# Kernel optimization log

Hardware: AMD Instinct MI355X
Metric: run time of the kernel (lower is better)

The kernel has to match this reference:

```python
import jax, jax.numpy as jnp
import numpy as np

NUM_INPUTS = 4096
K = 64
BATCH = 16384


def setup_inputs() -> dict:
    key = jax.random.key(0)
    X = jax.random.normal(key, (BATCH, NUM_INPUTS), dtype=jnp.float32)
    return {"X": X}


def reference(X):
    # Per-row (1 - k/n) quantile of |X| (linear interpolation, matching
    # torch.quantile default), then soft-threshold preserving sign.
    q = 1.0 - K / NUM_INPUTS
    X_abs = jnp.abs(X)
    Q = jnp.quantile(X_abs, q, axis=1, method="linear")  # [batch]
    X_trunc = jnp.maximum(X_abs - Q[:, None], 0.0)
    return jnp.sign(X) * X_trunc
```

## Files before the change

kernel.cpp:

```cpp
#include <hip/hip_runtime.h>
#include <cstdint>

constexpr int NCOLS   = 4096;
constexpr int THREADS = 256;
constexpr int EPT     = NCOLS / THREADS;
constexpr int KSEL    = 65;
constexpr uint32_t TPAT = 0x40000000u;
constexpr int CAP     = 256;

typedef float f32x4 __attribute__((ext_vector_type(4)));

__device__ __forceinline__ float soft(float x, float Q) {
    float r = fmaxf(fabsf(x) - Q, 0.0f);
    return copysignf(r, x);
}

__global__ __launch_bounds__(THREADS) void topk_sparsify(
    const float* __restrict__ X, float* __restrict__ out, int rows)
{
    const int row = blockIdx.x;
    if (row >= rows) return;
    const int t    = threadIdx.x;
    const int lane = t & 63;
    const int wave = t >> 6;

    const f32x4* __restrict__ x4 = reinterpret_cast<const f32x4*>(X + (size_t)row * NCOLS);
    f32x4* __restrict__       o4 = reinterpret_cast<f32x4*>(out + (size_t)row * NCOLS);

    f32x4 d[4];
#pragma unroll
    for (int i = 0; i < 4; ++i) d[i] = __builtin_nontemporal_load(x4 + t + THREADS * i);

    uint32_t a[EPT];
#pragma unroll
    for (int i = 0; i < 4; ++i) {
#pragma unroll
        for (int j = 0; j < 4; ++j)
            a[4 * i + j] = __float_as_uint(d[i][j]) & 0x7FFFFFFFu;
    }

    __shared__ uint32_t list[CAP];
    __shared__ uint32_t wtot[4];
    __shared__ uint32_t wcnt[4], wmn[4];
    __shared__ uint32_t b65_s;
    __shared__ float    q_sh;

    uint32_t cnt = 0;
#pragma unroll
    for (int i = 0; i < EPT; ++i) cnt += (a[i] > TPAT) ? 1u : 0u;

    uint32_t inc = cnt;
#pragma unroll
    for (int off = 1; off < 64; off <<= 1) {
        uint32_t v = __shfl_up(inc, off, 64);
        if (lane >= off) inc += v;
    }
    if (lane == 63) wtot[wave] = inc;
    __syncthreads();

    uint32_t C = 0, base = 0;
#pragma unroll
    for (int w = 0; w < 4; ++w) {
        uint32_t tw = wtot[w];
        C += tw;
        if (w < wave) base += tw;
    }
    const bool fast = (C >= (uint32_t)KSEL) && (C <= (uint32_t)CAP);

    if (fast) {
        uint32_t o = base + inc - cnt;
#pragma unroll
        for (int i = 0; i < EPT; ++i)
            if (a[i] > TPAT) list[o++] = a[i];
    }
    __syncthreads();

    uint32_t b65;
    if (fast) {
        if (t < 64) {
            const uint32_t c0 = ((uint32_t)t        < C) ? list[t]        : 0u;
            const uint32_t c1 = ((uint32_t)t + 64u  < C) ? list[t + 64]   : 0u;
            const uint32_t c2 = ((uint32_t)t + 128u < C) ? list[t + 128]  : 0u;
            const uint32_t c3 = ((uint32_t)t + 192u < C) ? list[t + 192]  : 0u;
            uint32_t prefix = 0, kk = KSEL;
            for (int b = 30; b >= 0; --b) {
                const uint32_t want = prefix | (1u << b);
                const uint32_t mhi  = ~((1u << b) - 1u);
                uint64_t m0 = __ballot((c0 & mhi) == want);
                uint64_t m1 = __ballot((c1 & mhi) == want);
                uint64_t m2 = __ballot((c2 & mhi) == want);
                uint64_t m3 = __ballot((c3 & mhi) == want);
                const uint32_t cc = (uint32_t)(__popcll(m0) + __popcll(m1) +
                                               __popcll(m2) + __popcll(m3));
                if (cc >= kk) prefix = want; else kk -= cc;
            }
            if (t == 0) b65_s = prefix;
        }
        __syncthreads();
        b65 = b65_s;
    } else {
        uint32_t prefix = 0, kk = KSEL;
        for (int b = 30; b >= 0; --b) {
            const uint32_t want = prefix | (1u << b);
            const uint32_t mhi  = ~((1u << b) - 1u);
            uint32_t c = 0;
#pragma unroll
            for (int i = 0; i < EPT; ++i) c += ((a[i] & mhi) == want) ? 1u : 0u;
#pragma unroll
            for (int off2 = 32; off2 >= 1; off2 >>= 1) c += __shfl_down(c, off2, 64);
            if (lane == 0) wcnt[wave] = c;
            __syncthreads();
            const uint32_t tot = wcnt[0] + wcnt[1] + wcnt[2] + wcnt[3];
            if (tot >= kk) prefix = want; else kk -= tot;
            __syncthreads();
        }
        b65 = prefix;
    }
    const float v65 = __uint_as_float(b65);

    uint32_t cgt = 0, mn = 0xFFFFFFFFu;
#pragma unroll
    for (int i = 0; i < EPT; ++i) {
        if (a[i] > b65) { cgt++; mn = min(mn, a[i]); }
    }
#pragma unroll
    for (int off2 = 32; off2 >= 1; off2 >>= 1) {
        cgt += __shfl_down(cgt, off2, 64);
        uint32_t m2 = __shfl_down(mn, off2, 64);
        mn = min(mn, m2);
    }
    if (lane == 0) { wcnt[wave] = cgt; wmn[wave] = mn; }
    __syncthreads();
    if (t == 0) {
        const uint32_t Ct = wcnt[0] + wcnt[1] + wcnt[2] + wcnt[3];
        const uint32_t M  = min(min(wmn[0], wmn[1]), min(wmn[2], wmn[3]));
        const float v64 = (Ct == 64u) ? __uint_as_float(M) : v65;
        q_sh = fmaf(0.015625f, v64 - v65, v65);
    }
    __syncthreads();
    const float Q = q_sh;

#pragma unroll
    for (int i = 0; i < 4; ++i) {
        f32x4 f;
#pragma unroll
        for (int j = 0; j < 4; ++j) f[j] = soft(d[i][j], Q);
        __builtin_nontemporal_store(f, o4 + t + THREADS * i);
    }
}

extern "C" void kernel_launch(void* const* d_in, const int* in_sizes, int n_in,
                              void* d_out, int out_size, void* d_ws, size_t ws_size,
                              hipStream_t stream) {
    const float* X   = (const float*)d_in[0];
    float*       out = (float*)d_out;
    const int rows = in_sizes[0] / NCOLS;
    topk_sparsify<<<rows, THREADS, 0, stream>>>(X, out, rows);
}
```

Measured before the change: 411.8 us.

## Drop raw input registers via sign bitmask and fold v64 search into fast path

Measured after the change: 410.6 us. About the same (-0.3%).

```diff
diff --git a/kernel.cpp b/kernel.cpp
--- a/kernel.cpp
+++ b/kernel.cpp
@@ -10,12 +10,7 @@
 
 typedef float f32x4 __attribute__((ext_vector_type(4)));
 
-__device__ __forceinline__ float soft(float x, float Q) {
-    float r = fmaxf(fabsf(x) - Q, 0.0f);
-    return copysignf(r, x);
-}
-
-__global__ __launch_bounds__(THREADS) void topk_sparsify(
+__global__ __launch_bounds__(THREADS, 8) void topk_sparsify(
     const float* __restrict__ X, float* __restrict__ out, int rows)
 {
     const int row = blockIdx.x;
@@ -25,24 +20,23 @@
     const int wave = t >> 6;
 
     const f32x4* __restrict__ x4 = reinterpret_cast<const f32x4*>(X + (size_t)row * NCOLS);
-    f32x4* __restrict__       o4 = reinterpret_cast<f32x4*>(out + (size_t)row * NCOLS);
-
-    f32x4 d[4];
-#pragma unroll
-    for (int i = 0; i < 4; ++i) d[i] = __builtin_nontemporal_load(x4 + t + THREADS * i);
 
     uint32_t a[EPT];
+    uint32_t smask = 0;
 #pragma unroll
     for (int i = 0; i < 4; ++i) {
+        f32x4 v = __builtin_nontemporal_load(x4 + t + THREADS * i);
 #pragma unroll
-        for (int j = 0; j < 4; ++j)
-            a[4 * i + j] = __float_as_uint(d[i][j]) & 0x7FFFFFFFu;
+        for (int j = 0; j < 4; ++j) {
+            const uint32_t p = __float_as_uint(v[j]);
+            smask |= (p >> 31) << (4 * i + j);
+            a[4 * i + j] = p & 0x7FFFFFFFu;
+        }
     }
 
     __shared__ uint32_t list[CAP];
     __shared__ uint32_t wtot[4];
     __shared__ uint32_t wcnt[4], wmn[4];
-    __shared__ uint32_t b65_s;
     __shared__ float    q_sh;
 
     uint32_t cnt = 0;
@@ -61,7 +55,7 @@
     uint32_t C = 0, base = 0;
 #pragma unroll
     for (int w = 0; w < 4; ++w) {
-        uint32_t tw = wtot[w];
+        const uint32_t tw = wtot[w];
         C += tw;
         if (w < wave) base += tw;
     }
@@ -72,33 +66,46 @@
 #pragma unroll
         for (int i = 0; i < EPT; ++i)
             if (a[i] > TPAT) list[o++] = a[i];
-    }
-    __syncthreads();
+        __syncthreads();
 
-    uint32_t b65;
-    if (fast) {
         if (t < 64) {
-            const uint32_t c0 = ((uint32_t)t        < C) ? list[t]        : 0u;
-            const uint32_t c1 = ((uint32_t)t + 64u  < C) ? list[t + 64]   : 0u;
-            const uint32_t c2 = ((uint32_t)t + 128u < C) ? list[t + 128]  : 0u;
-            const uint32_t c3 = ((uint32_t)t + 192u < C) ? list[t + 192]  : 0u;
+            const uint32_t c0 = ((uint32_t)t        < C) ? list[t]       : 0u;
+            const uint32_t c1 = ((uint32_t)t + 64u  < C) ? list[t + 64]  : 0u;
+            const uint32_t c2 = ((uint32_t)t + 128u < C) ? list[t + 128] : 0u;
+            const uint32_t c3 = ((uint32_t)t + 192u < C) ? list[t + 192] : 0u;
             uint32_t prefix = 0, kk = KSEL;
             for (int b = 30; b >= 0; --b) {
                 const uint32_t want = prefix | (1u << b);
                 const uint32_t mhi  = ~((1u << b) - 1u);
-                uint64_t m0 = __ballot((c0 & mhi) == want);
-                uint64_t m1 = __ballot((c1 & mhi) == want);
-                uint64_t m2 = __ballot((c2 & mhi) == want);
-                uint64_t m3 = __ballot((c3 & mhi) == want);
+                const uint64_t m0 = __ballot((c0 & mhi) == want);
+                const uint64_t m1 = __ballot((c1 & mhi) == want);
+                const uint64_t m2 = __ballot((c2 & mhi) == want);
+                const uint64_t m3 = __ballot((c3 & mhi) == want);
                 const uint32_t cc = (uint32_t)(__popcll(m0) + __popcll(m1) +
                                                __popcll(m2) + __popcll(m3));
                 if (cc >= kk) prefix = want; else kk -= cc;
             }
-            if (t == 0) b65_s = prefix;
+            const uint32_t cgt = (uint32_t)(__popcll(__ballot(c0 > prefix)) +
+                                            __popcll(__ballot(c1 > prefix)) +
+                                            __popcll(__ballot(c2 > prefix)) +
+                                            __popcll(__ballot(c3 > prefix)));
+            uint32_t mnl = 0xFFFFFFFFu;
+            if (c0 > prefix) mnl = min(mnl, c0);
+            if (c1 > prefix) mnl = min(mnl, c1);
+            if (c2 > prefix) mnl = min(mnl, c2);
+            if (c3 > prefix) mnl = min(mnl, c3);
+#pragma unroll
+            for (int off = 32; off >= 1; off >>= 1)
+                mnl = min(mnl, (uint32_t)__shfl_xor(mnl, off, 64));
+            if (t == 0) {
+                const float v65 = __uint_as_float(prefix);
+                const float v64 = (cgt == 64u) ? __uint_as_float(mnl) : v65;
+                q_sh = fmaf(0.015625f, v64 - v65, v65);
+            }
         }
         __syncthreads();
-        b65 = b65_s;
     } else {
+        __syncthreads();
         uint32_t prefix = 0, kk = KSEL;
         for (int b = 30; b >= 0; --b) {
             const uint32_t want = prefix | (1u << b);
@@ -114,37 +121,41 @@
             if (tot >= kk) prefix = want; else kk -= tot;
             __syncthreads();
         }
-        b65 = prefix;
+        uint32_t cgt = 0, mn = 0xFFFFFFFFu;
+#pragma unroll
+        for (int i = 0; i < EPT; ++i) {
+            if (a[i] > prefix) { cgt++; mn = min(mn, a[i]); }
+        }
+#pragma unroll
+        for (int off2 = 32; off2 >= 1; off2 >>= 1) {
+            cgt += __shfl_down(cgt, off2, 64);
+            const uint32_t m2 = __shfl_down(mn, off2, 64);
+            mn = min(mn, m2);
+        }
+        if (lane == 0) { wcnt[wave] = cgt; wmn[wave] = mn; }
+        __syncthreads();
+        if (t == 0) {
+            const uint32_t Ct = wcnt[0] + wcnt[1] + wcnt[2] + wcnt[3];
+            const uint32_t M  = min(min(wmn[0], wmn[1]), min(wmn[2], wmn[3]));
+            const float v65 = __uint_as_float(prefix);
+            const float v64 = (Ct == 64u) ? __uint_as_float(M) : v65;
+            q_sh = fmaf(0.015625f, v64 - v65, v65);
+        }
+        __syncthreads();
     }
-    const float v65 = __uint_as_float(b65);
-
-    uint32_t cgt = 0, mn = 0xFFFFFFFFu;
-#pragma unroll
-    for (int i = 0; i < EPT; ++i) {
-        if (a[i] > b65) { cgt++; mn = min(mn, a[i]); }
-    }
-#pragma unroll
-    for (int off2 = 32; off2 >= 1; off2 >>= 1) {
-        cgt += __shfl_down(cgt, off2, 64);
-        uint32_t m2 = __shfl_down(mn, off2, 64);
-        mn = min(mn, m2);
-    }
-    if (lane == 0) { wcnt[wave] = cgt; wmn[wave] = mn; }
-    __syncthreads();
-    if (t == 0) {
-        const uint32_t Ct = wcnt[0] + wcnt[1] + wcnt[2] + wcnt[3];
-        const uint32_t M  = min(min(wmn[0], wmn[1]), min(wmn[2], wmn[3]));
-        const float v64 = (Ct == 64u) ? __uint_as_float(M) : v65;
-        q_sh = fmaf(0.015625f, v64 - v65, v65);
-    }
-    __syncthreads();
     const float Q = q_sh;
 
+    f32x4* __restrict__ o4 = reinterpret_cast<f32x4*>(out + (size_t)row * NCOLS);
 #pragma unroll
     for (int i = 0; i < 4; ++i) {
         f32x4 f;
 #pragma unroll
-        for (int j = 0; j < 4; ++j) f[j] = soft(d[i][j], Q);
+        for (int j = 0; j < 4; ++j) {
+            const int e = 4 * i + j;
+            const float r = fmaxf(__uint_as_float(a[e]) - Q, 0.0f);
+            const uint32_t sp = __float_as_uint(r) | ((smask << (31 - e)) & 0x80000000u);
+            f[j] = __uint_as_float(sp);
+        }
         __builtin_nontemporal_store(f, o4 + t + THREADS * i);
     }
 }
```
